# Optimization experiments

Measured on AMD Instinct MI355X. Metric: run time of the kernel, lower is better.

Reference implementation:

```python
import jax, jax.numpy as jnp
import numpy as np

B, L, D, N = 4, 8192, 128, 32


def setup_inputs() -> dict:
    key = jax.random.key(0)
    ks = jax.random.split(key, 12)
    s = 0.05  # small init scale for stability of exp/cumsum
    return {
        "x": jax.random.normal(ks[0], (B, L, D), jnp.float32),
        "h_t_minus_1": jax.random.normal(ks[1], (B, L, D), jnp.float32),
        "A_log": jax.random.normal(ks[2], (D, N), jnp.float32),
        "D_param": jnp.ones((D,), jnp.float32),
        "W_x": jax.random.normal(ks[3], (D, 2 * N + D), jnp.float32) * s,
        "W_dt": jax.random.normal(ks[4], (D, D), jnp.float32) * s,
        "b_dt": jnp.zeros((D,), jnp.float32),
        "conv_w": jax.random.normal(ks[5], (3, D, D), jnp.float32) * s,  # (width, in, out)
        "conv_b": jnp.zeros((D,), jnp.float32),
        "W_f": jax.random.normal(ks[6], (D, D), jnp.float32) * s,
        "b_f": jnp.zeros((D,), jnp.float32),
    }


def reference(x, h_t_minus_1, A_log, D_param, W_x, W_dt, b_dt, conv_w, conv_b, W_f, b_f):
    d, n = A_log.shape
    A = -jnp.exp(A_log)  # (d, n)
    x_dbl = x @ W_x  # (b, l, d + 2n)
    delta, Bm, Cm = jnp.split(x_dbl, [d, d + n], axis=-1)
    delta = jax.nn.softplus(delta @ W_dt + b_dt)  # (b, l, d)

    # selective scan
    dA = jnp.einsum('bld,dn->bldn', delta, A)
    dB_u = jnp.einsum('bld,bld,bln->bldn', delta, h_t_minus_1, Bm)
    dA_cumsum = jnp.exp(jnp.cumsum(dA, axis=1) - dA)  # exclusive cumsum
    h_t = jnp.einsum('bldn,bln->bld', dB_u * dA_cumsum, Cm)
    h_t = h_t + h_t * D_param

    ssm_output = jax.nn.relu(h_t @ W_f + b_f)
    # causal Conv1D, kernel=3: left-pad by 2
    conv = jax.lax.conv_general_dilated(
        ssm_output, conv_w, window_strides=(1,), padding=[(2, 0)],
        dimension_numbers=('NWC', 'WIO', 'NWC')) + conv_b
    causal_output = jax.nn.relu(conv)
    fused_output = ssm_output * causal_output
    return (fused_output, h_t)
```

## Files before the change

kernel.cpp:

```cpp
#include <hip/hip_runtime.h>
#include <math.h>

typedef unsigned short u16;
typedef __attribute__((ext_vector_type(8))) short short8v;
typedef __attribute__((ext_vector_type(4))) float f32x4;

constexpr int B_  = 4;
constexpr int L_  = 8192;
constexpr int D_  = 128;
constexpr int N_  = 32;
constexpr int BL  = B_ * L_;
constexpr int CH  = 16;
constexpr int NC  = L_ / CH;

__device__ inline unsigned bfr(float x) {
    unsigned u = __float_as_uint(x);
    return (u + 0x7fffu + ((u >> 16) & 1u)) >> 16;
}
__device__ inline unsigned pkbf(float a, float b) { return bfr(a) | (bfr(b) << 16); }
__device__ inline float b2f(u16 h) { return __uint_as_float(((unsigned)h) << 16); }

__global__ __launch_bounds__(512) void prep_weff(
    const float* __restrict__ Wx, const float* __restrict__ Wdt,
    u16* __restrict__ Wt0)
{
    __shared__ float wd[128 * 128];
    const int tid = threadIdx.x;
    #pragma unroll
    for (int j = 0; j < 8; ++j) {
        const int g = tid + j * 512;
        *reinterpret_cast<float4*>(&wd[g * 4]) =
            *reinterpret_cast<const float4*>(&Wdt[(size_t)g * 4]);
    }
    __syncthreads();
    const int k = blockIdx.x * 4 + (tid >> 7);
    const int d = tid & 127;
    float s = 0.f;
    #pragma unroll 8
    for (int j = 0; j < 128; ++j)
        s = fmaf(Wx[(size_t)k * 192 + j], wd[j * 128 + d], s);
    Wt0[d * 128 + k] = (u16)bfr(s);
}

__global__ __launch_bounds__(256) void prep_rest(
    const float* __restrict__ Wx, const float* __restrict__ Wf,
    const float* __restrict__ Wconv, const float* __restrict__ A_log,
    u16* __restrict__ Wt0, u16* __restrict__ Wt2, u16* __restrict__ Wtc,
    float* __restrict__ negA)
{
    const int which = blockIdx.y;
    const int t = blockIdx.x * 256 + threadIdx.x;
    if (which == 0) {
        if (t >= 64 * 128) return;
        const int n = t >> 7, k = t & 127;
        Wt0[(128 + n) * 128 + k] = (u16)bfr(Wx[(size_t)k * 192 + 128 + n]);
    } else if (which == 1) {
        if (t >= 128 * 128) return;
        const int n = t >> 7, k = t & 127;
        Wt2[n * 128 + k] = (u16)bfr(Wf[(size_t)k * 128 + n]);
    } else if (which <= 4) {
        if (t >= 128 * 128) return;
        const int w = which - 2;
        const int n = t >> 7, k = t & 127;
        Wtc[((size_t)w * 128 + n) * 128 + k] = (u16)bfr(Wconv[((size_t)w * 128 + k) * 128 + n]);
    } else {
        if (t < D_ * N_) negA[t] = -expf(A_log[t]) * 1.4426950408889634f;
    }
}

__global__ __launch_bounds__(256) void gemm1(
    const float* __restrict__ x, const u16* __restrict__ Wt0,
    const float* __restrict__ b_dt,
    float* __restrict__ delta, float* __restrict__ Sloc,
    float* __restrict__ bc, float* __restrict__ part)
{
    __shared__ __align__(16) u16 Blds[192 * 128];

    const int tid = threadIdx.x;
    const int r0 = blockIdx.x * 64;

    #pragma unroll
    for (int j = 0; j < 12; ++j) {
        const int g = tid + j * 256;
        const int n = g >> 4, k8 = (g & 15) * 8;
        const uint4 p = *reinterpret_cast<const uint4*>(&Wt0[(size_t)n * 128 + k8]);
        *reinterpret_cast<uint4*>(&Blds[n * 128 + (k8 ^ ((n & 7) << 3))]) = p;
    }

    const int w = tid >> 6, lane = tid & 63;
    const int lr = lane & 15, kg = lane >> 4;
    const int arow = r0 + w * 16 + lr;

    float4 av[4][2];
    #pragma unroll
    for (int ks = 0; ks < 4; ++ks) {
        const float* src = &x[(size_t)arow * 128 + ks * 32 + kg * 8];
        av[ks][0] = *reinterpret_cast<const float4*>(src);
        av[ks][1] = *reinterpret_cast<const float4*>(src + 4);
    }
    __syncthreads();

    f32x4 acc[12] = {};
    #pragma unroll
    for (int ks = 0; ks < 4; ++ks) {
        uint4 ap;
        ap.x = pkbf(av[ks][0].x, av[ks][0].y);
        ap.y = pkbf(av[ks][0].z, av[ks][0].w);
        ap.z = pkbf(av[ks][1].x, av[ks][1].y);
        ap.w = pkbf(av[ks][1].z, av[ks][1].w);
        const short8v af = *reinterpret_cast<const short8v*>(&ap);
        const int kb = ks * 32 + kg * 8;
        #pragma unroll
        for (int nf = 0; nf < 12; ++nf) {
            const int n = nf * 16 + lr;
            const short8v bf = *reinterpret_cast<const short8v*>(
                &Blds[n * 128 + (kb ^ ((n & 7) << 3))]);
            acc[nf] = __builtin_amdgcn_mfma_f32_16x16x32_bf16(af, bf, acc[nf], 0, 0, 0);
        }
    }

    const int orow = r0 + w * 16;
    const size_t chunkb = (size_t)(orow / CH) * 128;
    #pragma unroll
    for (int nf = 0; nf < 8; ++nf) {
        const int col = nf * 16 + lr;
        const float bb = b_dt[col];
        float v[4];
        #pragma unroll
        for (int q = 0; q < 4; ++q) {
            const float t = acc[nf][q] + bb;
            v[q] = fmaxf(t, 0.f) + log1pf(expf(-fabsf(t)));
        }
        const float e1 = v[0], e2 = e1 + v[1], e3 = e2 + v[2];
        const float g4 = e3 + v[3];
        const float g0 = __shfl(g4, lr, 64);
        const float g1 = __shfl(g4, lr + 16, 64);
        const float g2 = __shfl(g4, lr + 32, 64);
        const float g3 = __shfl(g4, lr + 48, 64);
        float base = 0.f;
        if (kg > 0) base += g0;
        if (kg > 1) base += g1;
        if (kg > 2) base += g2;
        const size_t rb = (size_t)(orow + kg * 4) * 128 + col;
        delta[rb + 0 * 128] = v[0];
        delta[rb + 1 * 128] = v[1];
        delta[rb + 2 * 128] = v[2];
        delta[rb + 3 * 128] = v[3];
        Sloc[rb + 0 * 128] = base;
        Sloc[rb + 1 * 128] = base + e1;
        Sloc[rb + 2 * 128] = base + e2;
        Sloc[rb + 3 * 128] = base + e3;
        if (kg == 0) part[chunkb + col] = g0 + g1 + g2 + g3;
    }
    #pragma unroll
    for (int h = 0; h < 2; ++h)
        #pragma unroll
        for (int q = 0; q < 4; ++q)
            bc[(size_t)(orow + kg * 4 + q) * 32 + h * 16 + lr] =
                acc[8 + h][q] * acc[10 + h][q];
}

__global__ __launch_bounds__(512) void scan_prefix(float* __restrict__ part)
{
    const int b = blockIdx.x, d = blockIdx.y;
    const int c = threadIdx.x, w = c >> 6, lane = c & 63;
    const size_t idx = ((size_t)b * NC + c) * 128 + d;
    const float v = part[idx];
    float s = v;
    #pragma unroll
    for (int off = 1; off < 64; off <<= 1) {
        const float t = __shfl_up(s, off, 64);
        if (lane >= off) s += t;
    }
    __shared__ float wsum[8];
    if (lane == 63) wsum[w] = s;
    __syncthreads();
    float add = 0.f;
    #pragma unroll
    for (int i = 0; i < 8; ++i)
        if (i < w) add += wsum[i];
    part[idx] = s + add - v;
}

__global__ __launch_bounds__(512) void scan_h(
    const float* __restrict__ delta, const float* __restrict__ Sloc,
    const float* __restrict__ hprev, const float* __restrict__ bc,
    const float* __restrict__ negA, const float* __restrict__ Dp,
    const float* __restrict__ part,
    float* __restrict__ h_out, u16* __restrict__ hb)
{
    const int tid = threadIdx.x;
    const int d = tid & 127;
    float a[N_];
    #pragma unroll
    for (int n4 = 0; n4 < 8; ++n4) {
        const float4 v = *reinterpret_cast<const float4*>(&negA[d * N_ + n4 * 4]);
        a[n4 * 4 + 0] = v.x; a[n4 * 4 + 1] = v.y;
        a[n4 * 4 + 2] = v.z; a[n4 * 4 + 3] = v.w;
    }
    const float dp1 = 1.f + Dp[d];

    #pragma unroll
    for (int it = 0; it < 4; ++it) {
        const size_t row = ((size_t)blockIdx.x + (size_t)it * 2048) * 4 + (tid >> 7);
        const size_t rb = row * 128 + d;
        const float dv = delta[rb];
        const float sl = Sloc[rb];
        const float hv = hprev[rb];
        const float S = part[(row >> 4) * 128 + d] + sl;
        float p0 = 0.f, p1 = 0.f, p2 = 0.f, p3 = 0.f;
        #pragma unroll
        for (int n4 = 0; n4 < 8; ++n4) {
            const float4 b4 = *reinterpret_cast<const float4*>(&bc[row * 32 + n4 * 4]);
            p0 = fmaf(b4.x, exp2f(S * a[n4 * 4 + 0]), p0);
            p1 = fmaf(b4.y, exp2f(S * a[n4 * 4 + 1]), p1);
            p2 = fmaf(b4.z, exp2f(S * a[n4 * 4 + 2]), p2);
            p3 = fmaf(b4.w, exp2f(S * a[n4 * 4 + 3]), p3);
        }
        const float h = dv * hv * ((p0 + p1) + (p2 + p3)) * dp1;
        h_out[rb] = h;
        hb[rb] = (u16)bfr(h);
    }
}

__global__ __launch_bounds__(256) void conv_fuse2(
    const u16* __restrict__ hb, const u16* __restrict__ Wt2,
    const float* __restrict__ b_f, const u16* __restrict__ Wtc,
    const float* __restrict__ cbias, float* __restrict__ fused)
{
    __shared__ __align__(16) u16 hb_s[80 * 128];
    __shared__ __align__(16) u16 ssm_s[80 * 128];

    const int tid = threadIdx.x;
    const int bb = blockIdx.y;
    const int r0 = blockIdx.x * 64;
    const u16* hbB = hb + (size_t)bb * L_ * 128;

    #pragma unroll
    for (int j = 0; j < 5; ++j) {
        const int g = tid + j * 256;
        const int s = g >> 4, k8 = (g & 15) * 8;
        const int grow = r0 - 2 + s;
        uint4 p = make_uint4(0, 0, 0, 0);
        if (grow >= 0 && grow < L_)
            p = *reinterpret_cast<const uint4*>(&hbB[(size_t)grow * 128 + k8]);
        *reinterpret_cast<uint4*>(&hb_s[s * 128 + (k8 ^ ((s & 7) << 3))]) = p;
    }
    __syncthreads();

    const int w = tid >> 6, lane = tid & 63;
    const int lr = lane & 15, kg = lane >> 4;

    for (int sm = w; sm < 5; sm += 4) {
        f32x4 acc[8] = {};
        #pragma unroll
        for (int ks = 0; ks < 4; ++ks) {
            const int kb = ks * 32 + kg * 8;
            const int sr = sm * 16 + lr;
            const short8v af = *reinterpret_cast<const short8v*>(
                &hb_s[sr * 128 + (kb ^ ((sr & 7) << 3))]);
            #pragma unroll
            for (int nf = 0; nf < 8; ++nf) {
                const int col = nf * 16 + lr;
                const short8v bf = *reinterpret_cast<const short8v*>(
                    &Wt2[(size_t)col * 128 + kb]);
                acc[nf] = __builtin_amdgcn_mfma_f32_16x16x32_bf16(af, bf, acc[nf], 0, 0, 0);
            }
        }
        #pragma unroll
        for (int nf = 0; nf < 8; ++nf) {
            const int col = nf * 16 + lr;
            const float bbv = b_f[col];
            #pragma unroll
            for (int q = 0; q < 4; ++q) {
                const int s2 = sm * 16 + kg * 4 + q;
                float vv = fmaxf(acc[nf][q] + bbv, 0.f);
                if (r0 - 2 + s2 < 0) vv = 0.f;
                ssm_s[s2 * 128 + (col ^ ((s2 & 7) << 3))] = (u16)bfr(vv);
            }
        }
    }
    __syncthreads();

    f32x4 acc[8] = {};
    #pragma unroll
    for (int ks = 0; ks < 4; ++ks) {
        const int kb = ks * 32 + kg * 8;
        short8v af[3];
        #pragma unroll
        for (int t = 0; t < 3; ++t) {
            const int sr = w * 16 + lr + t;
            af[t] = *reinterpret_cast<const short8v*>(
                &ssm_s[sr * 128 + (kb ^ ((sr & 7) << 3))]);
        }
        #pragma unroll
        for (int nf = 0; nf < 8; ++nf) {
            const int col = nf * 16 + lr;
            #pragma unroll
            for (int t = 0; t < 3; ++t) {
                const short8v bf = *reinterpret_cast<const short8v*>(
                    &Wtc[((size_t)t * 128 + col) * 128 + kb]);
                acc[nf] = __builtin_amdgcn_mfma_f32_16x16x32_bf16(af[t], bf, acc[nf], 0, 0, 0);
            }
        }
    }
    #pragma unroll
    for (int nf = 0; nf < 8; ++nf) {
        const int col = nf * 16 + lr;
        const float cbv = cbias[col];
        #pragma unroll
        for (int q = 0; q < 4; ++q) {
            const int ro = w * 16 + kg * 4 + q;
            const int s2 = ro + 2;
            const u16 sv = ssm_s[s2 * 128 + (col ^ ((s2 & 7) << 3))];
            const float cv = fmaxf(acc[nf][q] + cbv, 0.f);
            fused[((size_t)bb * L_ + r0 + ro) * 128 + col] = b2f(sv) * cv;
        }
    }
}

extern "C" void kernel_launch(void* const* d_in, const int* in_sizes, int n_in,
                              void* d_out, int out_size, void* d_ws, size_t ws_size,
                              hipStream_t stream)
{
    const float* x      = (const float*)d_in[0];
    const float* hprev  = (const float*)d_in[1];
    const float* A_log  = (const float*)d_in[2];
    const float* Dp     = (const float*)d_in[3];
    const float* W_x    = (const float*)d_in[4];
    const float* W_dt   = (const float*)d_in[5];
    const float* b_dt   = (const float*)d_in[6];
    const float* conv_w = (const float*)d_in[7];
    const float* conv_b = (const float*)d_in[8];
    const float* W_f    = (const float*)d_in[9];
    const float* b_f    = (const float*)d_in[10];

    float* out   = (float*)d_out;
    float* h_out = out + (size_t)BL * D_;

    char* ws = (char*)d_ws;
    float* delta = (float*)ws;                  ws += (size_t)BL * 128 * 4;
    float* sloc  = (float*)ws;                  ws += (size_t)BL * 128 * 4;
    float* bcb   = (float*)ws;                  ws += (size_t)BL * 32 * 4;
    float* part  = (float*)ws;                  ws += (size_t)B_ * NC * 128 * 4;
    float* negA  = (float*)ws;                  ws += (size_t)D_ * N_ * 4;
    u16*   Wt0   = (u16*)ws;                    ws += (size_t)192 * 128 * 2;
    u16*   Wt2   = (u16*)ws;                    ws += (size_t)128 * 128 * 2;
    u16*   Wtc   = (u16*)ws;                    ws += (size_t)3 * 128 * 128 * 2;
    u16*   hb    = (u16*)ws;

    prep_weff<<<dim3(32), dim3(512), 0, stream>>>(W_x, W_dt, Wt0);
    prep_rest<<<dim3(64, 6), dim3(256), 0, stream>>>(
        W_x, W_f, conv_w, A_log, Wt0, Wt2, Wtc, negA);
    gemm1<<<dim3(BL / 64), dim3(256), 0, stream>>>(
        x, Wt0, b_dt, delta, sloc, bcb, part);
    scan_prefix<<<dim3(B_, D_), dim3(512), 0, stream>>>(part);
    scan_h<<<dim3(2048), dim3(512), 0, stream>>>(
        delta, sloc, hprev, bcb, negA, Dp, part, h_out, hb);
    conv_fuse2<<<dim3(L_ / 64, B_), dim3(256), 0, stream>>>(
        hb, Wt2, b_f, Wtc, conv_b, out);
}
```

Measured before the change: 198.5 us.

## Skip underflowing scan terms and fuse W_f GEMM into scan kernel

The scan kernel now works on 32-row chunks per block and loads the transposed A matrix and B/C values into LDS. A per-wave `__any` test skips the 32 exp2 evaluations when every d in the wave has S*max(A) below -80, because those terms underflow to essentially zero. The W_f GEMM with ReLU is moved into the scan kernel, and the bf16 ssm output is written directly. The conv kernel then only loads ssm rows with a 2-row halo instead of recomputing the projection for 80 rows. The skip drops contributions at the 2^-80 level, and the tiles are now smaller per block.

```diff
diff --git a/kernel.cpp b/kernel.cpp
--- a/kernel.cpp
+++ b/kernel.cpp
@@ -12,6 +12,8 @@
 constexpr int BL  = B_ * L_;
 constexpr int CH  = 16;
 constexpr int NC  = L_ / CH;
+constexpr int SCH = 32;
+constexpr int SNC = L_ / SCH;
 
 __device__ inline unsigned bfr(float x) {
     unsigned u = __float_as_uint(x);
@@ -46,10 +48,11 @@
     const float* __restrict__ Wx, const float* __restrict__ Wf,
     const float* __restrict__ Wconv, const float* __restrict__ A_log,
     u16* __restrict__ Wt0, u16* __restrict__ Wt2, u16* __restrict__ Wtc,
-    float* __restrict__ negA)
+    float* __restrict__ negAT, float* __restrict__ amax)
 {
     const int which = blockIdx.y;
     const int t = blockIdx.x * 256 + threadIdx.x;
+    constexpr float L2E = 1.4426950408889634f;
     if (which == 0) {
         if (t >= 64 * 128) return;
         const int n = t >> 7, k = t & 127;
@@ -63,8 +66,16 @@
         const int w = which - 2;
         const int n = t >> 7, k = t & 127;
         Wtc[((size_t)w * 128 + n) * 128 + k] = (u16)bfr(Wconv[((size_t)w * 128 + k) * 128 + n]);
+    } else if (which == 5) {
+        if (t >= 128 * 32) return;
+        const int d = t >> 5, n = t & 31;
+        negAT[n * 128 + d] = -expf(A_log[d * 32 + n]) * L2E;
     } else {
-        if (t < D_ * N_) negA[t] = -expf(A_log[t]) * 1.4426950408889634f;
+        if (t >= 128) return;
+        float m = -1e30f;
+        for (int n = 0; n < 32; ++n)
+            m = fmaxf(m, -expf(A_log[t * 32 + n]) * L2E);
+        amax[t] = m;
     }
 }
 
@@ -182,140 +193,161 @@
     part[idx] = s + add - v;
 }
 
-__global__ __launch_bounds__(512) void scan_h(
+__global__ __launch_bounds__(512) void scan_main(
     const float* __restrict__ delta, const float* __restrict__ Sloc,
     const float* __restrict__ hprev, const float* __restrict__ bc,
-    const float* __restrict__ negA, const float* __restrict__ Dp,
-    const float* __restrict__ part,
-    float* __restrict__ h_out, u16* __restrict__ hb)
-{
+    const float* __restrict__ negAT, const float* __restrict__ amax,
+    const float* __restrict__ Dp, const float* __restrict__ part,
+    const u16* __restrict__ Wt2, const float* __restrict__ b_f,
+    float* __restrict__ h_out, u16* __restrict__ ssm)
+{
+    __shared__ float at_s[32 * 128];
+    __shared__ float bc_s[SCH * 32];
+    __shared__ __align__(16) u16 h_s[SCH * 128];
+
+    const int cb = blockIdx.x, b = blockIdx.y;
     const int tid = threadIdx.x;
-    const int d = tid & 127;
-    float a[N_];
-    #pragma unroll
-    for (int n4 = 0; n4 < 8; ++n4) {
-        const float4 v = *reinterpret_cast<const float4*>(&negA[d * N_ + n4 * 4]);
-        a[n4 * 4 + 0] = v.x; a[n4 * 4 + 1] = v.y;
-        a[n4 * 4 + 2] = v.z; a[n4 * 4 + 3] = v.w;
-    }
+    const size_t rowbase = (size_t)b * L_ + (size_t)cb * SCH;
+
+    #pragma unroll
+    for (int j = 0; j < 2; ++j) {
+        const int g = tid + j * 512;
+        reinterpret_cast<float4*>(at_s)[g] =
+            reinterpret_cast<const float4*>(negAT)[g];
+    }
+    if (tid < 256)
+        reinterpret_cast<float4*>(bc_s)[tid] =
+            reinterpret_cast<const float4*>(&bc[rowbase * 32])[tid];
+
+    const int d = tid & 127, r0 = tid >> 7;
     const float dp1 = 1.f + Dp[d];
-
-    #pragma unroll
-    for (int it = 0; it < 4; ++it) {
-        const size_t row = ((size_t)blockIdx.x + (size_t)it * 2048) * 4 + (tid >> 7);
-        const size_t rb = row * 128 + d;
-        const float dv = delta[rb];
-        const float sl = Sloc[rb];
-        const float hv = hprev[rb];
-        const float S = part[(row >> 4) * 128 + d] + sl;
-        float p0 = 0.f, p1 = 0.f, p2 = 0.f, p3 = 0.f;
-        #pragma unroll
-        for (int n4 = 0; n4 < 8; ++n4) {
-            const float4 b4 = *reinterpret_cast<const float4*>(&bc[row * 32 + n4 * 4]);
-            p0 = fmaf(b4.x, exp2f(S * a[n4 * 4 + 0]), p0);
-            p1 = fmaf(b4.y, exp2f(S * a[n4 * 4 + 1]), p1);
-            p2 = fmaf(b4.z, exp2f(S * a[n4 * 4 + 2]), p2);
-            p3 = fmaf(b4.w, exp2f(S * a[n4 * 4 + 3]), p3);
-        }
-        const float h = dv * hv * ((p0 + p1) + (p2 + p3)) * dp1;
+    const float am = amax[d];
+    const size_t pbase = ((size_t)b * NC + (size_t)cb * 2) * 128 + d;
+    const float part0 = part[pbase];
+    const float part1 = part[pbase + 128];
+    __syncthreads();
+
+    for (int r = 0; r < 8; ++r) {
+        const int i = r * 4 + r0;
+        const size_t rb = (rowbase + i) * 128 + d;
+        const float S = ((i < 16) ? part0 : part1) + Sloc[rb];
+        float h = 0.f;
+        const int need = (S * am >= -80.f);
+        if (__any(need)) {
+            const float dv = delta[rb];
+            const float hv = hprev[rb];
+            float p0 = 0.f, p1 = 0.f, p2 = 0.f, p3 = 0.f;
+            #pragma unroll
+            for (int n4 = 0; n4 < 8; ++n4) {
+                const float4 b4 = *reinterpret_cast<const float4*>(&bc_s[i * 32 + n4 * 4]);
+                p0 = fmaf(b4.x, exp2f(S * at_s[(n4 * 4 + 0) * 128 + d]), p0);
+                p1 = fmaf(b4.y, exp2f(S * at_s[(n4 * 4 + 1) * 128 + d]), p1);
+                p2 = fmaf(b4.z, exp2f(S * at_s[(n4 * 4 + 2) * 128 + d]), p2);
+                p3 = fmaf(b4.w, exp2f(S * at_s[(n4 * 4 + 3) * 128 + d]), p3);
+            }
+            h = dv * hv * ((p0 + p1) + (p2 + p3)) * dp1;
+        }
         h_out[rb] = h;
-        hb[rb] = (u16)bfr(h);
-    }
-}
-
-__global__ __launch_bounds__(256) void conv_fuse2(
-    const u16* __restrict__ hb, const u16* __restrict__ Wt2,
-    const float* __restrict__ b_f, const u16* __restrict__ Wtc,
+        h_s[i * 128 + (((d >> 3) ^ (i & 7)) << 3) + (d & 7)] = (u16)bfr(h);
+    }
+    __syncthreads();
+
+    const int wid = tid >> 6, lane = tid & 63;
+    const int lr = lane & 15, kg = lane >> 4;
+    const int col = wid * 16 + lr;
+    f32x4 acc[2] = {};
+    #pragma unroll
+    for (int ks = 0; ks < 4; ++ks) {
+        const int k8 = ks * 32 + kg * 8;
+        const short8v bfg = *reinterpret_cast<const short8v*>(&Wt2[(size_t)col * 128 + k8]);
+        #pragma unroll
+        for (int m = 0; m < 2; ++m) {
+            const int row = m * 16 + lr;
+            const short8v afg = *reinterpret_cast<const short8v*>(
+                &h_s[row * 128 + (k8 ^ ((row & 7) << 3))]);
+            acc[m] = __builtin_amdgcn_mfma_f32_16x16x32_bf16(afg, bfg, acc[m], 0, 0, 0);
+        }
+    }
+    const float bb = b_f[col];
+    #pragma unroll
+    for (int m = 0; m < 2; ++m)
+        #pragma unroll
+        for (int q = 0; q < 4; ++q) {
+            const int row = m * 16 + kg * 4 + q;
+            const float v = fmaxf(acc[m][q] + bb, 0.f);
+            ssm[(rowbase + row) * 128 + col] = (u16)bfr(v);
+        }
+}
+
+__global__ __launch_bounds__(512) void conv_fuse(
+    const u16* __restrict__ ssm, const u16* __restrict__ Wtc,
     const float* __restrict__ cbias, float* __restrict__ fused)
 {
-    __shared__ __align__(16) u16 hb_s[80 * 128];
-    __shared__ __align__(16) u16 ssm_s[80 * 128];
+    __shared__ __align__(16) u16 Alds[66 * 128];
 
     const int tid = threadIdx.x;
     const int bb = blockIdx.y;
     const int r0 = blockIdx.x * 64;
-    const u16* hbB = hb + (size_t)bb * L_ * 128;
-
-    #pragma unroll
-    for (int j = 0; j < 5; ++j) {
-        const int g = tid + j * 256;
-        const int s = g >> 4, k8 = (g & 15) * 8;
-        const int grow = r0 - 2 + s;
-        uint4 p = make_uint4(0, 0, 0, 0);
-        if (grow >= 0 && grow < L_)
-            p = *reinterpret_cast<const uint4*>(&hbB[(size_t)grow * 128 + k8]);
-        *reinterpret_cast<uint4*>(&hb_s[s * 128 + (k8 ^ ((s & 7) << 3))]) = p;
-    }
-    __syncthreads();
-
-    const int w = tid >> 6, lane = tid & 63;
+    const u16* sb = ssm + (size_t)bb * L_ * 128;
+
+    #pragma unroll
+    for (int j = 0; j < 3; ++j) {
+        const int g = tid + j * 512;
+        if (g < 66 * 16) {
+            const int i = g >> 4, k8 = (g & 15) * 8;
+            const int gr = r0 - 2 + i;
+            uint4 p = make_uint4(0, 0, 0, 0);
+            if (gr >= 0)
+                p = *reinterpret_cast<const uint4*>(&sb[(size_t)gr * 128 + k8]);
+            *reinterpret_cast<uint4*>(&Alds[i * 128 + (k8 ^ ((i & 7) << 3))]) = p;
+        }
+    }
+    __syncthreads();
+
+    const int wid = tid >> 6, lane = tid & 63;
+    const int wm = wid >> 2, wn = wid & 3;
     const int lr = lane & 15, kg = lane >> 4;
 
-    for (int sm = w; sm < 5; sm += 4) {
-        f32x4 acc[8] = {};
-        #pragma unroll
-        for (int ks = 0; ks < 4; ++ks) {
-            const int kb = ks * 32 + kg * 8;
-            const int sr = sm * 16 + lr;
-            const short8v af = *reinterpret_cast<const short8v*>(
-                &hb_s[sr * 128 + (kb ^ ((sr & 7) << 3))]);
+    f32x4 acc[2][2] = {};
+    #pragma unroll
+    for (int ks = 0; ks < 4; ++ks) {
+        const int k8 = ks * 32 + kg * 8;
+        short8v af[2][3];
+        #pragma unroll
+        for (int m = 0; m < 2; ++m)
             #pragma unroll
-            for (int nf = 0; nf < 8; ++nf) {
-                const int col = nf * 16 + lr;
-                const short8v bf = *reinterpret_cast<const short8v*>(
-                    &Wt2[(size_t)col * 128 + kb]);
-                acc[nf] = __builtin_amdgcn_mfma_f32_16x16x32_bf16(af, bf, acc[nf], 0, 0, 0);
+            for (int w = 0; w < 3; ++w) {
+                const int ri = wm * 32 + m * 16 + lr + w;
+                af[m][w] = *reinterpret_cast<const short8v*>(
+                    &Alds[ri * 128 + (k8 ^ ((ri & 7) << 3))]);
             }
-        }
-        #pragma unroll
-        for (int nf = 0; nf < 8; ++nf) {
-            const int col = nf * 16 + lr;
-            const float bbv = b_f[col];
+        #pragma unroll
+        for (int nf = 0; nf < 2; ++nf) {
+            const int col = wn * 32 + nf * 16 + lr;
+            #pragma unroll
+            for (int w = 0; w < 3; ++w) {
+                const short8v bfg = *reinterpret_cast<const short8v*>(
+                    &Wtc[((size_t)w * 128 + col) * 128 + k8]);
+                acc[0][nf] = __builtin_amdgcn_mfma_f32_16x16x32_bf16(af[0][w], bfg, acc[0][nf], 0, 0, 0);
+                acc[1][nf] = __builtin_amdgcn_mfma_f32_16x16x32_bf16(af[1][w], bfg, acc[1][nf], 0, 0, 0);
+            }
+        }
+    }
+
+    #pragma unroll
+    for (int nf = 0; nf < 2; ++nf) {
+        const int col = wn * 32 + nf * 16 + lr;
+        const float bb2 = cbias[col];
+        #pragma unroll
+        for (int m = 0; m < 2; ++m)
             #pragma unroll
             for (int q = 0; q < 4; ++q) {
-                const int s2 = sm * 16 + kg * 4 + q;
-                float vv = fmaxf(acc[nf][q] + bbv, 0.f);
-                if (r0 - 2 + s2 < 0) vv = 0.f;
-                ssm_s[s2 * 128 + (col ^ ((s2 & 7) << 3))] = (u16)bfr(vv);
+                const int row = wm * 32 + m * 16 + kg * 4 + q;
+                const int ri = row + 2;
+                const u16 sh = Alds[ri * 128 + ((((col >> 3) ^ (ri & 7)) << 3)) + (col & 7)];
+                const float cv = fmaxf(acc[m][nf][q] + bb2, 0.f);
+                fused[((size_t)bb * L_ + r0 + row) * 128 + col] = b2f(sh) * cv;
             }
-        }
-    }
-    __syncthreads();
-
-    f32x4 acc[8] = {};
-    #pragma unroll
-    for (int ks = 0; ks < 4; ++ks) {
-        const int kb = ks * 32 + kg * 8;
-        short8v af[3];
-        #pragma unroll
-        for (int t = 0; t < 3; ++t) {
-            const int sr = w * 16 + lr + t;
-            af[t] = *reinterpret_cast<const short8v*>(
-                &ssm_s[sr * 128 + (kb ^ ((sr & 7) << 3))]);
-        }
-        #pragma unroll
-        for (int nf = 0; nf < 8; ++nf) {
-            const int col = nf * 16 + lr;
-            #pragma unroll
-            for (int t = 0; t < 3; ++t) {
-                const short8v bf = *reinterpret_cast<const short8v*>(
-                    &Wtc[((size_t)t * 128 + col) * 128 + kb]);
-                acc[nf] = __builtin_amdgcn_mfma_f32_16x16x32_bf16(af[t], bf, acc[nf], 0, 0, 0);
-            }
-        }
-    }
-    #pragma unroll
-    for (int nf = 0; nf < 8; ++nf) {
-        const int col = nf * 16 + lr;
-        const float cbv = cbias[col];
-        #pragma unroll
-        for (int q = 0; q < 4; ++q) {
-            const int ro = w * 16 + kg * 4 + q;
-            const int s2 = ro + 2;
-            const u16 sv = ssm_s[s2 * 128 + (col ^ ((s2 & 7) << 3))];
-            const float cv = fmaxf(acc[nf][q] + cbv, 0.f);
-            fused[((size_t)bb * L_ + r0 + ro) * 128 + col] = b2f(sv) * cv;
-        }
     }
 }
 
@@ -343,20 +375,21 @@
     float* sloc  = (float*)ws;                  ws += (size_t)BL * 128 * 4;
     float* bcb   = (float*)ws;                  ws += (size_t)BL * 32 * 4;
     float* part  = (float*)ws;                  ws += (size_t)B_ * NC * 128 * 4;
-    float* negA  = (float*)ws;                  ws += (size_t)D_ * N_ * 4;
+    float* negAT = (float*)ws;                  ws += (size_t)N_ * 128 * 4;
+    float* amaxb = (float*)ws;                  ws += (size_t)128 * 4;
     u16*   Wt0   = (u16*)ws;                    ws += (size_t)192 * 128 * 2;
     u16*   Wt2   = (u16*)ws;                    ws += (size_t)128 * 128 * 2;
     u16*   Wtc   = (u16*)ws;                    ws += (size_t)3 * 128 * 128 * 2;
-    u16*   hb    = (u16*)ws;
+    u16*   ssm   = (u16*)ws;
 
     prep_weff<<<dim3(32), dim3(512), 0, stream>>>(W_x, W_dt, Wt0);
-    prep_rest<<<dim3(64, 6), dim3(256), 0, stream>>>(
-        W_x, W_f, conv_w, A_log, Wt0, Wt2, Wtc, negA);
+    prep_rest<<<dim3(64, 7), dim3(256), 0, stream>>>(
+        W_x, W_f, conv_w, A_log, Wt0, Wt2, Wtc, negAT, amaxb);
     gemm1<<<dim3(BL / 64), dim3(256), 0, stream>>>(
         x, Wt0, b_dt, delta, sloc, bcb, part);
     scan_prefix<<<dim3(B_, D_), dim3(512), 0, stream>>>(part);
-    scan_h<<<dim3(2048), dim3(512), 0, stream>>>(
-        delta, sloc, hprev, bcb, negA, Dp, part, h_out, hb);
-    conv_fuse2<<<dim3(L_ / 64, B_), dim3(256), 0, stream>>>(
-        hb, Wt2, b_f, Wtc, conv_b, out);
-}
+    scan_main<<<dim3(SNC, B_), dim3(512), 0, stream>>>(
+        delta, sloc, hprev, bcb, negAT, amaxb, Dp, part, Wt2, b_f, h_out, ssm);
+    conv_fuse<<<dim3(L_ / 64, B_), dim3(512), 0, stream>>>(
+        ssm, Wtc, conv_b, out);
+}
```

Measured after the change: 171.5 us. 1.16x faster.

## Fuse GEMM, chunk scan, h computation and conv into one cooperative kernel

Applied to the files above, without the earlier changes.

Replaces the separate gemm1, scan_prefix, scan_h and conv_fuse2 launches with a single cooperative kernel of 256 blocks of 128 rows each. Stages are separated by grid.sync, and delta, B*C and h stay in LDS instead of going through global workspace. Only the two boundary ssm rows per block pass through global memory for the causal conv halo. It also adds a per-d max of A, used to skip the 32-term exp2 sum for whole wavefronts whose cumulative decay has underflowed. The costs are grid-wide barriers, a large 128KB LDS footprint that needs every block co-resident, Wt0 read straight from global in the GEMM, and the skip approximating tiny contributions as zero.

```diff
diff --git a/kernel.cpp b/kernel.cpp
--- a/kernel.cpp
+++ b/kernel.cpp
@@ -1,17 +1,22 @@
 #include <hip/hip_runtime.h>
+#include <hip/hip_cooperative_groups.h>
 #include <math.h>
+
+namespace cg = cooperative_groups;
 
 typedef unsigned short u16;
 typedef __attribute__((ext_vector_type(8))) short short8v;
 typedef __attribute__((ext_vector_type(4))) float f32x4;
 
-constexpr int B_  = 4;
-constexpr int L_  = 8192;
-constexpr int D_  = 128;
-constexpr int N_  = 32;
-constexpr int BL  = B_ * L_;
-constexpr int CH  = 16;
-constexpr int NC  = L_ / CH;
+constexpr int B_   = 4;
+constexpr int L_   = 8192;
+constexpr int D_   = 128;
+constexpr int N_   = 32;
+constexpr int BL   = B_ * L_;
+constexpr int CH   = 16;
+constexpr int NC   = L_ / CH;
+constexpr int ROWS = 128;
+constexpr int NBLK = BL / ROWS;
 
 __device__ inline unsigned bfr(float x) {
     unsigned u = __float_as_uint(x);
@@ -46,10 +51,11 @@
     const float* __restrict__ Wx, const float* __restrict__ Wf,
     const float* __restrict__ Wconv, const float* __restrict__ A_log,
     u16* __restrict__ Wt0, u16* __restrict__ Wt2, u16* __restrict__ Wtc,
-    float* __restrict__ negA)
+    float* __restrict__ negAT, float* __restrict__ amax)
 {
     const int which = blockIdx.y;
     const int t = blockIdx.x * 256 + threadIdx.x;
+    constexpr float L2E = 1.4426950408889634f;
     if (which == 0) {
         if (t >= 64 * 128) return;
         const int n = t >> 7, k = t & 127;
@@ -63,207 +69,191 @@
         const int w = which - 2;
         const int n = t >> 7, k = t & 127;
         Wtc[((size_t)w * 128 + n) * 128 + k] = (u16)bfr(Wconv[((size_t)w * 128 + k) * 128 + n]);
+    } else if (which == 5) {
+        if (t >= 128 * 32) return;
+        const int d = t >> 5, n = t & 31;
+        negAT[n * 128 + d] = -expf(A_log[d * 32 + n]) * L2E;
     } else {
-        if (t < D_ * N_) negA[t] = -expf(A_log[t]) * 1.4426950408889634f;
-    }
-}
-
-__global__ __launch_bounds__(256) void gemm1(
-    const float* __restrict__ x, const u16* __restrict__ Wt0,
-    const float* __restrict__ b_dt,
-    float* __restrict__ delta, float* __restrict__ Sloc,
-    float* __restrict__ bc, float* __restrict__ part)
+        if (t >= 128) return;
+        float m = -1e30f;
+        for (int n = 0; n < 32; ++n)
+            m = fmaxf(m, -expf(A_log[t * 32 + n]) * L2E);
+        amax[t] = m;
+    }
+}
+
+__global__ __launch_bounds__(512, 2) void mega(
+    const float* __restrict__ x, const float* __restrict__ hprev,
+    const u16* __restrict__ Wt0, const u16* __restrict__ Wt2,
+    const u16* __restrict__ Wtc,
+    const float* __restrict__ b_dt, const float* __restrict__ b_f,
+    const float* __restrict__ cbias,
+    const float* __restrict__ negAT, const float* __restrict__ amax,
+    const float* __restrict__ Dp,
+    float* __restrict__ part, u16* __restrict__ ssm,
+    float* __restrict__ h_out, float* __restrict__ fused)
 {
-    __shared__ __align__(16) u16 Blds[192 * 128];
-
+    __shared__ __align__(16) char smem[131072];
+    float* delta_s = (float*)smem;
+    float* bc_s    = (float*)(smem + 65536);
+    float* at_s    = (float*)(smem + 81920);
+    u16*   h_s     = (u16*)(smem + 98304);
+    u16*   ssm_s   = (u16*)smem;
+    __shared__ float wsum[8];
+
+    cg::grid_group grid = cg::this_grid();
     const int tid = threadIdx.x;
-    const int r0 = blockIdx.x * 64;
-
-    #pragma unroll
-    for (int j = 0; j < 12; ++j) {
-        const int g = tid + j * 256;
-        const int n = g >> 4, k8 = (g & 15) * 8;
-        const uint4 p = *reinterpret_cast<const uint4*>(&Wt0[(size_t)n * 128 + k8]);
-        *reinterpret_cast<uint4*>(&Blds[n * 128 + (k8 ^ ((n & 7) << 3))]) = p;
-    }
-
+    const int bid = blockIdx.x;
+    const int R0 = bid * ROWS;
     const int w = tid >> 6, lane = tid & 63;
     const int lr = lane & 15, kg = lane >> 4;
-    const int arow = r0 + w * 16 + lr;
-
-    float4 av[4][2];
-    #pragma unroll
-    for (int ks = 0; ks < 4; ++ks) {
-        const float* src = &x[(size_t)arow * 128 + ks * 32 + kg * 8];
-        av[ks][0] = *reinterpret_cast<const float4*>(src);
-        av[ks][1] = *reinterpret_cast<const float4*>(src + 4);
+
+    {
+        const int arow = R0 + w * 16 + lr;
+        float4 av[4][2];
+        #pragma unroll
+        for (int ks = 0; ks < 4; ++ks) {
+            const float* src = &x[(size_t)arow * 128 + ks * 32 + kg * 8];
+            av[ks][0] = *reinterpret_cast<const float4*>(src);
+            av[ks][1] = *reinterpret_cast<const float4*>(src + 4);
+        }
+        f32x4 acc[12] = {};
+        #pragma unroll
+        for (int ks = 0; ks < 4; ++ks) {
+            uint4 ap;
+            ap.x = pkbf(av[ks][0].x, av[ks][0].y);
+            ap.y = pkbf(av[ks][0].z, av[ks][0].w);
+            ap.z = pkbf(av[ks][1].x, av[ks][1].y);
+            ap.w = pkbf(av[ks][1].z, av[ks][1].w);
+            const short8v af = *reinterpret_cast<const short8v*>(&ap);
+            const int kb = ks * 32 + kg * 8;
+            #pragma unroll
+            for (int nf = 0; nf < 12; ++nf) {
+                const int n = nf * 16 + lr;
+                const short8v bf = *reinterpret_cast<const short8v*>(
+                    &Wt0[(size_t)n * 128 + kb]);
+                acc[nf] = __builtin_amdgcn_mfma_f32_16x16x32_bf16(af, bf, acc[nf], 0, 0, 0);
+            }
+        }
+        const int orowl = w * 16;
+        const size_t chunkb = (size_t)((R0 + orowl) >> 4) * 128;
+        #pragma unroll
+        for (int nf = 0; nf < 8; ++nf) {
+            const int col = nf * 16 + lr;
+            const float bb = b_dt[col];
+            float v[4];
+            #pragma unroll
+            for (int q = 0; q < 4; ++q) {
+                const float t = acc[nf][q] + bb;
+                v[q] = fmaxf(t, 0.f) + log1pf(expf(-fabsf(t)));
+            }
+            const float g4 = v[0] + v[1] + v[2] + v[3];
+            const float g0 = __shfl(g4, lr, 64);
+            const float g1 = __shfl(g4, lr + 16, 64);
+            const float g2 = __shfl(g4, lr + 32, 64);
+            const float g3 = __shfl(g4, lr + 48, 64);
+            const int rl = orowl + kg * 4;
+            delta_s[(rl + 0) * 128 + col] = v[0];
+            delta_s[(rl + 1) * 128 + col] = v[1];
+            delta_s[(rl + 2) * 128 + col] = v[2];
+            delta_s[(rl + 3) * 128 + col] = v[3];
+            if (kg == 0) part[chunkb + col] = g0 + g1 + g2 + g3;
+        }
+        #pragma unroll
+        for (int h2 = 0; h2 < 2; ++h2)
+            #pragma unroll
+            for (int q = 0; q < 4; ++q)
+                bc_s[(orowl + kg * 4 + q) * 32 + h2 * 16 + lr] =
+                    acc[8 + h2][q] * acc[10 + h2][q];
+    }
+    __threadfence();
+    grid.sync();
+
+    #pragma unroll 1
+    for (int si = 0; si < 2; ++si) {
+        const int s = bid * 2 + si;
+        const int b = s >> 7, d = s & 127;
+        const size_t idx = ((size_t)b * NC + tid) * 128 + d;
+        const float v = part[idx];
+        float sc = v;
+        #pragma unroll
+        for (int off = 1; off < 64; off <<= 1) {
+            const float t = __shfl_up(sc, off, 64);
+            if (lane >= off) sc += t;
+        }
+        if (lane == 63) wsum[w] = sc;
+        __syncthreads();
+        float add = 0.f;
+        #pragma unroll
+        for (int i2 = 0; i2 < 8; ++i2)
+            if (i2 < w) add += wsum[i2];
+        part[idx] = sc + add - v;
+        __syncthreads();
+    }
+    __threadfence();
+    grid.sync();
+
+    {
+        #pragma unroll
+        for (int j = 0; j < 2; ++j) {
+            const int g = tid + j * 512;
+            reinterpret_cast<float4*>(at_s)[g] =
+                reinterpret_cast<const float4*>(negAT)[g];
+        }
+        __syncthreads();
+        const int d = tid & 127, r0 = tid >> 7;
+        const float dp1 = 1.f + Dp[d];
+        const float am = amax[d];
+        #pragma unroll 1
+        for (int cc = 0; cc < 8; ++cc) {
+            float s = part[(size_t)((R0 >> 4) + cc) * 128 + d];
+            float sv[4];
+            #pragma unroll
+            for (int i = 0; i < 16; ++i) {
+                if ((i & 3) == r0) sv[i >> 2] = s;
+                s += delta_s[(cc * 16 + i) * 128 + d];
+            }
+            #pragma unroll 1
+            for (int k = 0; k < 4; ++k) {
+                const int row = cc * 16 + k * 4 + r0;
+                const size_t rb = (size_t)(R0 + row) * 128 + d;
+                const float S = sv[k];
+                float h = 0.f;
+                if (__any(S * am >= -80.f)) {
+                    const float dv = delta_s[row * 128 + d];
+                    const float hv = hprev[rb];
+                    float p0 = 0.f, p1 = 0.f, p2 = 0.f, p3 = 0.f;
+                    #pragma unroll
+                    for (int n4 = 0; n4 < 8; ++n4) {
+                        const float4 b4 = *reinterpret_cast<const float4*>(
+                            &bc_s[row * 32 + n4 * 4]);
+                        p0 = fmaf(b4.x, exp2f(S * at_s[(n4 * 4 + 0) * 128 + d]), p0);
+                        p1 = fmaf(b4.y, exp2f(S * at_s[(n4 * 4 + 1) * 128 + d]), p1);
+                        p2 = fmaf(b4.z, exp2f(S * at_s[(n4 * 4 + 2) * 128 + d]), p2);
+                        p3 = fmaf(b4.w, exp2f(S * at_s[(n4 * 4 + 3) * 128 + d]), p3);
+                    }
+                    h = dv * hv * ((p0 + p1) + (p2 + p3)) * dp1;
+                }
+                h_out[rb] = h;
+                h_s[row * 128 + (d ^ ((row & 7) << 3))] = (u16)bfr(h);
+            }
+        }
     }
     __syncthreads();
 
-    f32x4 acc[12] = {};
-    #pragma unroll
-    for (int ks = 0; ks < 4; ++ks) {
-        uint4 ap;
-        ap.x = pkbf(av[ks][0].x, av[ks][0].y);
-        ap.y = pkbf(av[ks][0].z, av[ks][0].w);
-        ap.z = pkbf(av[ks][1].x, av[ks][1].y);
-        ap.w = pkbf(av[ks][1].z, av[ks][1].w);
-        const short8v af = *reinterpret_cast<const short8v*>(&ap);
-        const int kb = ks * 32 + kg * 8;
-        #pragma unroll
-        for (int nf = 0; nf < 12; ++nf) {
-            const int n = nf * 16 + lr;
-            const short8v bf = *reinterpret_cast<const short8v*>(
-                &Blds[n * 128 + (kb ^ ((n & 7) << 3))]);
-            acc[nf] = __builtin_amdgcn_mfma_f32_16x16x32_bf16(af, bf, acc[nf], 0, 0, 0);
-        }
-    }
-
-    const int orow = r0 + w * 16;
-    const size_t chunkb = (size_t)(orow / CH) * 128;
-    #pragma unroll
-    for (int nf = 0; nf < 8; ++nf) {
-        const int col = nf * 16 + lr;
-        const float bb = b_dt[col];
-        float v[4];
-        #pragma unroll
-        for (int q = 0; q < 4; ++q) {
-            const float t = acc[nf][q] + bb;
-            v[q] = fmaxf(t, 0.f) + log1pf(expf(-fabsf(t)));
-        }
-        const float e1 = v[0], e2 = e1 + v[1], e3 = e2 + v[2];
-        const float g4 = e3 + v[3];
-        const float g0 = __shfl(g4, lr, 64);
-        const float g1 = __shfl(g4, lr + 16, 64);
-        const float g2 = __shfl(g4, lr + 32, 64);
-        const float g3 = __shfl(g4, lr + 48, 64);
-        float base = 0.f;
-        if (kg > 0) base += g0;
-        if (kg > 1) base += g1;
-        if (kg > 2) base += g2;
-        const size_t rb = (size_t)(orow + kg * 4) * 128 + col;
-        delta[rb + 0 * 128] = v[0];
-        delta[rb + 1 * 128] = v[1];
-        delta[rb + 2 * 128] = v[2];
-        delta[rb + 3 * 128] = v[3];
-        Sloc[rb + 0 * 128] = base;
-        Sloc[rb + 1 * 128] = base + e1;
-        Sloc[rb + 2 * 128] = base + e2;
-        Sloc[rb + 3 * 128] = base + e3;
-        if (kg == 0) part[chunkb + col] = g0 + g1 + g2 + g3;
-    }
-    #pragma unroll
-    for (int h = 0; h < 2; ++h)
-        #pragma unroll
-        for (int q = 0; q < 4; ++q)
-            bc[(size_t)(orow + kg * 4 + q) * 32 + h * 16 + lr] =
-                acc[8 + h][q] * acc[10 + h][q];
-}
-
-__global__ __launch_bounds__(512) void scan_prefix(float* __restrict__ part)
-{
-    const int b = blockIdx.x, d = blockIdx.y;
-    const int c = threadIdx.x, w = c >> 6, lane = c & 63;
-    const size_t idx = ((size_t)b * NC + c) * 128 + d;
-    const float v = part[idx];
-    float s = v;
-    #pragma unroll
-    for (int off = 1; off < 64; off <<= 1) {
-        const float t = __shfl_up(s, off, 64);
-        if (lane >= off) s += t;
-    }
-    __shared__ float wsum[8];
-    if (lane == 63) wsum[w] = s;
-    __syncthreads();
-    float add = 0.f;
-    #pragma unroll
-    for (int i = 0; i < 8; ++i)
-        if (i < w) add += wsum[i];
-    part[idx] = s + add - v;
-}
-
-__global__ __launch_bounds__(512) void scan_h(
-    const float* __restrict__ delta, const float* __restrict__ Sloc,
-    const float* __restrict__ hprev, const float* __restrict__ bc,
-    const float* __restrict__ negA, const float* __restrict__ Dp,
-    const float* __restrict__ part,
-    float* __restrict__ h_out, u16* __restrict__ hb)
-{
-    const int tid = threadIdx.x;
-    const int d = tid & 127;
-    float a[N_];
-    #pragma unroll
-    for (int n4 = 0; n4 < 8; ++n4) {
-        const float4 v = *reinterpret_cast<const float4*>(&negA[d * N_ + n4 * 4]);
-        a[n4 * 4 + 0] = v.x; a[n4 * 4 + 1] = v.y;
-        a[n4 * 4 + 2] = v.z; a[n4 * 4 + 3] = v.w;
-    }
-    const float dp1 = 1.f + Dp[d];
-
-    #pragma unroll
-    for (int it = 0; it < 4; ++it) {
-        const size_t row = ((size_t)blockIdx.x + (size_t)it * 2048) * 4 + (tid >> 7);
-        const size_t rb = row * 128 + d;
-        const float dv = delta[rb];
-        const float sl = Sloc[rb];
-        const float hv = hprev[rb];
-        const float S = part[(row >> 4) * 128 + d] + sl;
-        float p0 = 0.f, p1 = 0.f, p2 = 0.f, p3 = 0.f;
-        #pragma unroll
-        for (int n4 = 0; n4 < 8; ++n4) {
-            const float4 b4 = *reinterpret_cast<const float4*>(&bc[row * 32 + n4 * 4]);
-            p0 = fmaf(b4.x, exp2f(S * a[n4 * 4 + 0]), p0);
-            p1 = fmaf(b4.y, exp2f(S * a[n4 * 4 + 1]), p1);
-            p2 = fmaf(b4.z, exp2f(S * a[n4 * 4 + 2]), p2);
-            p3 = fmaf(b4.w, exp2f(S * a[n4 * 4 + 3]), p3);
-        }
-        const float h = dv * hv * ((p0 + p1) + (p2 + p3)) * dp1;
-        h_out[rb] = h;
-        hb[rb] = (u16)bfr(h);
-    }
-}
-
-__global__ __launch_bounds__(256) void conv_fuse2(
-    const u16* __restrict__ hb, const u16* __restrict__ Wt2,
-    const float* __restrict__ b_f, const u16* __restrict__ Wtc,
-    const float* __restrict__ cbias, float* __restrict__ fused)
-{
-    __shared__ __align__(16) u16 hb_s[80 * 128];
-    __shared__ __align__(16) u16 ssm_s[80 * 128];
-
-    const int tid = threadIdx.x;
-    const int bb = blockIdx.y;
-    const int r0 = blockIdx.x * 64;
-    const u16* hbB = hb + (size_t)bb * L_ * 128;
-
-    #pragma unroll
-    for (int j = 0; j < 5; ++j) {
-        const int g = tid + j * 256;
-        const int s = g >> 4, k8 = (g & 15) * 8;
-        const int grow = r0 - 2 + s;
-        uint4 p = make_uint4(0, 0, 0, 0);
-        if (grow >= 0 && grow < L_)
-            p = *reinterpret_cast<const uint4*>(&hbB[(size_t)grow * 128 + k8]);
-        *reinterpret_cast<uint4*>(&hb_s[s * 128 + (k8 ^ ((s & 7) << 3))]) = p;
-    }
-    __syncthreads();
-
-    const int w = tid >> 6, lane = tid & 63;
-    const int lr = lane & 15, kg = lane >> 4;
-
-    for (int sm = w; sm < 5; sm += 4) {
+    {
         f32x4 acc[8] = {};
         #pragma unroll
         for (int ks = 0; ks < 4; ++ks) {
-            const int kb = ks * 32 + kg * 8;
-            const int sr = sm * 16 + lr;
+            const int k8 = ks * 32 + kg * 8;
+            const int row = w * 16 + lr;
             const short8v af = *reinterpret_cast<const short8v*>(
-                &hb_s[sr * 128 + (kb ^ ((sr & 7) << 3))]);
+                &h_s[row * 128 + (k8 ^ ((row & 7) << 3))]);
             #pragma unroll
             for (int nf = 0; nf < 8; ++nf) {
                 const int col = nf * 16 + lr;
                 const short8v bf = *reinterpret_cast<const short8v*>(
-                    &Wt2[(size_t)col * 128 + kb]);
+                    &Wt2[(size_t)col * 128 + k8]);
                 acc[nf] = __builtin_amdgcn_mfma_f32_16x16x32_bf16(af, bf, acc[nf], 0, 0, 0);
             }
         }
@@ -273,48 +263,64 @@
             const float bbv = b_f[col];
             #pragma unroll
             for (int q = 0; q < 4; ++q) {
-                const int s2 = sm * 16 + kg * 4 + q;
-                float vv = fmaxf(acc[nf][q] + bbv, 0.f);
-                if (r0 - 2 + s2 < 0) vv = 0.f;
-                ssm_s[s2 * 128 + (col ^ ((s2 & 7) << 3))] = (u16)bfr(vv);
-            }
-        }
-    }
-    __syncthreads();
-
-    f32x4 acc[8] = {};
-    #pragma unroll
-    for (int ks = 0; ks < 4; ++ks) {
-        const int kb = ks * 32 + kg * 8;
-        short8v af[3];
-        #pragma unroll
-        for (int t = 0; t < 3; ++t) {
-            const int sr = w * 16 + lr + t;
-            af[t] = *reinterpret_cast<const short8v*>(
-                &ssm_s[sr * 128 + (kb ^ ((sr & 7) << 3))]);
+                const int row = w * 16 + kg * 4 + q;
+                const u16 sv16 = (u16)bfr(fmaxf(acc[nf][q] + bbv, 0.f));
+                const int ri = row + 2;
+                ssm_s[ri * 128 + (col ^ ((ri & 7) << 3))] = sv16;
+                if (row >= ROWS - 2)
+                    ssm[(size_t)(R0 + row) * 128 + col] = sv16;
+            }
+        }
+    }
+    __threadfence();
+    grid.sync();
+
+    {
+        if (tid < 32) {
+            const int i = tid >> 4, k8 = (tid & 15) * 8;
+            uint4 p = make_uint4(0, 0, 0, 0);
+            if ((bid & 63) != 0) {
+                const int gr = R0 - 2 + i;
+                p = *reinterpret_cast<const uint4*>(&ssm[(size_t)gr * 128 + k8]);
+            }
+            *reinterpret_cast<uint4*>(&ssm_s[i * 128 + (k8 ^ ((i & 7) << 3))]) = p;
+        }
+        __syncthreads();
+
+        f32x4 acc[8] = {};
+        #pragma unroll
+        for (int ks = 0; ks < 4; ++ks) {
+            const int k8 = ks * 32 + kg * 8;
+            short8v af[3];
+            #pragma unroll
+            for (int t = 0; t < 3; ++t) {
+                const int ri = w * 16 + lr + t;
+                af[t] = *reinterpret_cast<const short8v*>(
+                    &ssm_s[ri * 128 + (k8 ^ ((ri & 7) << 3))]);
+            }
+            #pragma unroll
+            for (int nf = 0; nf < 8; ++nf) {
+                const int col = nf * 16 + lr;
+                #pragma unroll
+                for (int t = 0; t < 3; ++t) {
+                    const short8v bf = *reinterpret_cast<const short8v*>(
+                        &Wtc[((size_t)t * 128 + col) * 128 + k8]);
+                    acc[nf] = __builtin_amdgcn_mfma_f32_16x16x32_bf16(af[t], bf, acc[nf], 0, 0, 0);
+                }
+            }
         }
         #pragma unroll
         for (int nf = 0; nf < 8; ++nf) {
             const int col = nf * 16 + lr;
-            #pragma unroll
-            for (int t = 0; t < 3; ++t) {
-                const short8v bf = *reinterpret_cast<const short8v*>(
-                    &Wtc[((size_t)t * 128 + col) * 128 + kb]);
-                acc[nf] = __builtin_amdgcn_mfma_f32_16x16x32_bf16(af[t], bf, acc[nf], 0, 0, 0);
-            }
-        }
-    }
-    #pragma unroll
-    for (int nf = 0; nf < 8; ++nf) {
-        const int col = nf * 16 + lr;
-        const float cbv = cbias[col];
-        #pragma unroll
-        for (int q = 0; q < 4; ++q) {
-            const int ro = w * 16 + kg * 4 + q;
-            const int s2 = ro + 2;
-            const u16 sv = ssm_s[s2 * 128 + (col ^ ((s2 & 7) << 3))];
-            const float cv = fmaxf(acc[nf][q] + cbv, 0.f);
-            fused[((size_t)bb * L_ + r0 + ro) * 128 + col] = b2f(sv) * cv;
+            const float cb = cbias[col];
+            #pragma unroll
+            for (int q = 0; q < 4; ++q) {
+                const int ro = w * 16 + kg * 4 + q;
+                const int ri = ro + 2;
+                const u16 sh = ssm_s[ri * 128 + (col ^ ((ri & 7) << 3))];
+                fused[(size_t)(R0 + ro) * 128 + col] =
+                    b2f(sh) * fmaxf(acc[nf][q] + cb, 0.f);
+            }
         }
     }
 }
@@ -339,24 +345,24 @@
     float* h_out = out + (size_t)BL * D_;
 
     char* ws = (char*)d_ws;
-    float* delta = (float*)ws;                  ws += (size_t)BL * 128 * 4;
-    float* sloc  = (float*)ws;                  ws += (size_t)BL * 128 * 4;
-    float* bcb   = (float*)ws;                  ws += (size_t)BL * 32 * 4;
     float* part  = (float*)ws;                  ws += (size_t)B_ * NC * 128 * 4;
-    float* negA  = (float*)ws;                  ws += (size_t)D_ * N_ * 4;
+    float* negAT = (float*)ws;                  ws += (size_t)N_ * 128 * 4;
+    float* amaxb = (float*)ws;                  ws += (size_t)128 * 4;
     u16*   Wt0   = (u16*)ws;                    ws += (size_t)192 * 128 * 2;
     u16*   Wt2   = (u16*)ws;                    ws += (size_t)128 * 128 * 2;
     u16*   Wtc   = (u16*)ws;                    ws += (size_t)3 * 128 * 128 * 2;
-    u16*   hb    = (u16*)ws;
+    u16*   ssm   = (u16*)ws;
 
     prep_weff<<<dim3(32), dim3(512), 0, stream>>>(W_x, W_dt, Wt0);
-    prep_rest<<<dim3(64, 6), dim3(256), 0, stream>>>(
-        W_x, W_f, conv_w, A_log, Wt0, Wt2, Wtc, negA);
-    gemm1<<<dim3(BL / 64), dim3(256), 0, stream>>>(
-        x, Wt0, b_dt, delta, sloc, bcb, part);
-    scan_prefix<<<dim3(B_, D_), dim3(512), 0, stream>>>(part);
-    scan_h<<<dim3(2048), dim3(512), 0, stream>>>(
-        delta, sloc, hprev, bcb, negA, Dp, part, h_out, hb);
-    conv_fuse2<<<dim3(L_ / 64, B_), dim3(256), 0, stream>>>(
-        hb, Wt2, b_f, Wtc, conv_b, out);
-}
+    prep_rest<<<dim3(64, 7), dim3(256), 0, stream>>>(
+        W_x, W_f, conv_w, A_log, Wt0, Wt2, Wtc, negAT, amaxb);
+
+    void* kargs[] = {
+        (void*)&x, (void*)&hprev, (void*)&Wt0, (void*)&Wt2, (void*)&Wtc,
+        (void*)&b_dt, (void*)&b_f, (void*)&conv_b, (void*)&negAT,
+        (void*)&amaxb, (void*)&Dp, (void*)&part, (void*)&ssm,
+        (void*)&h_out, (void*)&out
+    };
+    hipLaunchCooperativeKernel((const void*)mega, dim3(NBLK), dim3(512),
+                               kargs, 0, stream);
+}
```

Result: slower. 410.5 us (+106.8%).
